# Kernel optimization log

Hardware: AMD Instinct MI355X
Metric: run time of the kernel (lower is better)

## Reference

```python
import jax, jax.numpy as jnp
import numpy as np

NUM_RANGES = 31   # bins [0,1)...[29,30) plus [30, inf) -> max_height=30
EPS = 1e-06
ALPHA = 0.5
NAN_VALUE = -1.0


def setup_inputs() -> dict:
    key = jax.random.key(0)
    k1, k2 = jax.random.split(key)
    shape = (64, 512, 512)
    # targets in log1p space; natural heights expm1(target) span [0, ~34)
    target = jax.random.uniform(k1, shape, dtype=jnp.float32) * 3.55
    pred = target + 0.1 * jax.random.normal(k2, shape, dtype=jnp.float32)
    return {"pred": pred, "target": target}


def reference(pred, target):
    valid = target != NAN_VALUE                      # no-data mask
    natural = jnp.expm1(target)                      # heights in natural space
    # arithmetic bin index: ranges [i, i+1) for i<30, last bin [30, inf)
    bin_idx = jnp.clip(jnp.floor(natural), 0.0, NUM_RANGES - 1).astype(jnp.int32)
    in_range = natural >= 0.0                        # samples below 0 fall in no range

    # histogram of valid, in-range samples (scatter-add)
    counts = jnp.zeros(NUM_RANGES, jnp.float32).at[bin_idx.ravel()].add(
        (valid & in_range).ravel().astype(jnp.float32))
    total_valid = jnp.sum(valid).astype(jnp.float32)
    denom = jnp.maximum(total_valid, 1.0)
    freq = counts / denom
    w = 1.0 / (freq ** ALPHA + EPS)                  # inverse-frequency weights, [31]

    base = jnp.abs(pred - target)                    # L1 in log1p space
    sample_w = jnp.where(in_range, w[bin_idx], 0.0)  # gather per-sample weight
    weighted = base * sample_w
    # mean over valid samples (out-of-range valid samples contribute 0, as in torch)
    mean_loss = jnp.sum(jnp.where(valid, weighted, 0.0)) / denom
    return mean_loss
```

## Files before the change

### kernel.cpp

```cpp
#include <hip/hip_runtime.h>
#include <math.h>

#define NBINS 31
#define NSLOT 32
#define NCOPIES 256
#define BLOCK 256
#define GRID 768

#define CNT_SHIFT 25
#define SUM_MASK  0x1FFFFFFu
#define FIX_SCALE 32768.0f

typedef float f4 __attribute__((ext_vector_type(4)));


__device__ __forceinline__ void prep(float p, float t, unsigned hbase,
                                     unsigned& addr, unsigned& pk, unsigned& nvalid)
{
    nvalid += (t != -1.0f) ? 1u : 0u;
    bool ok = (t >= 0.0f);
    float nat = __expf(t) - 1.0f;
    unsigned b = (unsigned)(int)fminf(nat, 30.0f);
    unsigned pkv = (1u << CNT_SHIFT)
                 | (unsigned)(fabsf(p - t) * FIX_SCALE + 0.5f);
    pk   = ok ? pkv : 0u;
    addr = hbase + ((ok ? b : 31u) << 10);
}

__device__ __forceinline__ void packet(f4 p, f4 t, unsigned hbase,
                                       unsigned& nvalid)
{
    unsigned a0, a1, a2, a3, k0, k1, k2, k3;
    prep(p.x, t.x, hbase, a0, k0, nvalid);
    prep(p.y, t.y, hbase, a1, k1, nvalid);
    prep(p.z, t.z, hbase, a2, k2, nvalid);
    prep(p.w, t.w, hbase, a3, k3, nvalid);

    unsigned r0, r1, r2, r3;
    asm volatile(
        "ds_read_b32 %0, %4\n\t"
        "ds_read_b32 %1, %5\n\t"
        "ds_read_b32 %2, %6\n\t"
        "ds_read_b32 %3, %7"
        : "=&v"(r0), "=&v"(r1), "=&v"(r2), "=&v"(r3)
        : "v"(a0), "v"(a1), "v"(a2), "v"(a3));

    unsigned s0 = k0;
    unsigned s1 = k1 + (a1 == a0 ? s0 : 0u);
    unsigned s2 = k2 + (a2 == a1 ? s1 : (a2 == a0 ? s0 : 0u));
    unsigned s3 = k3 + (a3 == a2 ? s2 : (a3 == a1 ? s1 : (a3 == a0 ? s0 : 0u)));

    asm volatile(
        "s_waitcnt lgkmcnt(0)\n\t"
        "v_add_u32 %0, %0, %4\n\t"
        "v_add_u32 %1, %1, %5\n\t"
        "v_add_u32 %2, %2, %6\n\t"
        "v_add_u32 %3, %3, %7\n\t"
        "ds_write_b32 %8, %0\n\t"
        "ds_write_b32 %9, %1\n\t"
        "ds_write_b32 %10, %2\n\t"
        "ds_write_b32 %11, %3"
        : "+v"(r0), "+v"(r1), "+v"(r2), "+v"(r3)
        : "v"(s0), "v"(s1), "v"(s2), "v"(s3),
          "v"(a0), "v"(a1), "v"(a2), "v"(a3));
}

__device__ __forceinline__ void stage(unsigned* dst, const f4* p4, const f4* t4,
                                      int idx)
{
    __builtin_amdgcn_global_load_lds(
        (const __attribute__((address_space(1))) unsigned*)(const void*)(p4 + idx),
        (__attribute__((address_space(3))) unsigned*)dst, 16, 0, 0);
    __builtin_amdgcn_global_load_lds(
        (const __attribute__((address_space(1))) unsigned*)(const void*)(t4 + idx),
        (__attribute__((address_space(3))) unsigned*)(dst + 256), 16, 0, 0);
}

__device__ __forceinline__ void unstage(unsigned sa, f4& pv, f4& tv)
{
    asm volatile(
        "ds_read_b128 %0, %2\n\t"
        "ds_read_b128 %1, %2 offset:1024\n\t"
        "s_waitcnt lgkmcnt(0)"
        : "=&v"(pv), "=&v"(tv)
        : "v"(sa));
}

__global__ __launch_bounds__(BLOCK) void zero_ws_kernel(unsigned* ws)
{
    int t = threadIdx.x;
    if (t < 192) ws[t] = 0u;
}

__global__ __launch_bounds__(BLOCK, 3) void hist_kernel(
    const float* __restrict__ pred, const float* __restrict__ target, int n,
    float* __restrict__ g_sums, unsigned* __restrict__ g_cnts,
    unsigned* __restrict__ g_total)
{
    __shared__ unsigned s_hist[NSLOT * NCOPIES];
    __shared__ unsigned s_stage[2][BLOCK / 64][512];
    __shared__ float    p_sum[NBINS * 8];
    __shared__ unsigned p_cnt[NBINS * 8];
    __shared__ unsigned s_tot[BLOCK / 64];

    const int tid = threadIdx.x;
    {
        uint4 z = make_uint4(0u, 0u, 0u, 0u);
        uint4* h4 = (uint4*)s_hist;
        #pragma unroll
        for (int k = 0; k < (NSLOT * NCOPIES / 4) / BLOCK; ++k) h4[tid + k * BLOCK] = z;
    }
    __syncthreads();

    const unsigned hbase = (unsigned)(uintptr_t)(void*)s_hist + ((unsigned)tid << 2);
    const int lane = tid & 63, wv = tid >> 6;
    unsigned* stA = &s_stage[0][wv][0];
    unsigned* stB = &s_stage[1][wv][0];
    const unsigned saA = (unsigned)(uintptr_t)(void*)stA + ((unsigned)lane << 4);
    const unsigned saB = (unsigned)(uintptr_t)(void*)stB + ((unsigned)lane << 4);
    unsigned nvalid = 0;

    const int n4 = n >> 2;
    const f4* __restrict__ pred4 = (const f4*)pred;
    const f4* __restrict__ targ4 = (const f4*)target;
    const int st = GRID * BLOCK;
    const int i0 = blockIdx.x * BLOCK + tid;

    if ((n & 3) == 0 && (n4 & 63) == 0) {
        int i = i0;
        if (i < n4) {
            stage(stA, pred4, targ4, i);
            bool curA = true;
            for (; i + st < n4; i += st) {
                if (curA) stage(stB, pred4, targ4, i + st);
                else      stage(stA, pred4, targ4, i + st);
                asm volatile("s_waitcnt vmcnt(2)" ::: "memory");
                f4 pv, tv;
                unstage(curA ? saA : saB, pv, tv);
                packet(pv, tv, hbase, nvalid);
                curA = !curA;
            }
            asm volatile("s_waitcnt vmcnt(0)" ::: "memory");
            f4 pv, tv;
            unstage(curA ? saA : saB, pv, tv);
            packet(pv, tv, hbase, nvalid);
        }
    } else {
        for (int i = i0; i < n4; i += st) {
            f4 p = pred4[i];
            f4 t = targ4[i];
            packet(p, t, hbase, nvalid);
        }
        for (int i = (n4 << 2) + i0; i < n; i += st) {
            float p = pred[i], t = target[i];
            if (t != -1.0f) {
                atomicAdd(g_total, 1u);
                if (t >= 0.0f) {
                    float nat = __expf(t) - 1.0f;
                    int b = (int)fminf(nat, 30.0f);
                    atomicAdd(&g_sums[b], fabsf(p - t));
                    atomicAdd(&g_cnts[b], 1u);
                }
            }
        }
    }
    asm volatile("s_waitcnt lgkmcnt(0)" ::: "memory");
    __syncthreads();

    if (tid < NBINS * 8) {
        const int b = tid >> 3, g = tid & 7;
        const uint4* row = (const uint4*)(s_hist + b * NCOPIES);
        float fs = 0.0f; unsigned cs = 0u;
        #pragma unroll
        for (int kk = 0; kk < 8; ++kk) {
            uint4 v = row[g + 8 * kk];
            cs += (v.x >> CNT_SHIFT) + (v.y >> CNT_SHIFT)
                + (v.z >> CNT_SHIFT) + (v.w >> CNT_SHIFT);
            fs += (float)(v.x & SUM_MASK) + (float)(v.y & SUM_MASK)
                + (float)(v.z & SUM_MASK) + (float)(v.w & SUM_MASK);
        }
        p_sum[tid] = fs;
        p_cnt[tid] = cs;
    }
    unsigned v = nvalid;
    #pragma unroll
    for (int off = 32; off >= 1; off >>= 1) v += __shfl_down(v, off, 64);
    if ((tid & 63) == 0) s_tot[tid >> 6] = v;
    __syncthreads();

    if (tid < NBINS) {
        float fs = 0.0f; unsigned cs = 0u;
        #pragma unroll
        for (int g = 0; g < 8; ++g) { fs += p_sum[tid * 8 + g]; cs += p_cnt[tid * 8 + g]; }
        atomicAdd(&g_sums[tid], fs * (1.0f / FIX_SCALE));
        atomicAdd(&g_cnts[tid], cs);
    }
    if (tid == 0) {
        unsigned tot = 0;
        #pragma unroll
        for (int w = 0; w < BLOCK / 64; ++w) tot += s_tot[w];
        atomicAdd(g_total, tot);
    }
}

__global__ void finalize_kernel(const float* __restrict__ g_sums,
                                const unsigned* __restrict__ g_cnts,
                                const unsigned* __restrict__ g_total,
                                float* __restrict__ out)
{
    int lane = threadIdx.x;
    float denom = fmaxf((float)(*g_total), 1.0f);
    float contrib = 0.0f;
    if (lane < NBINS) {
        float freq = (float)g_cnts[lane] / denom;
        float w = 1.0f / (sqrtf(freq) + 1e-6f);
        contrib = g_sums[lane] * w;
    }
    #pragma unroll
    for (int off = 32; off >= 1; off >>= 1) contrib += __shfl_down(contrib, off, 64);
    if (lane == 0) *out = contrib / denom;
}

extern "C" void kernel_launch(void* const* d_in, const int* in_sizes, int n_in,
                              void* d_out, int out_size, void* d_ws, size_t ws_size,
                              hipStream_t stream)
{
    const float* pred   = (const float*)d_in[0];
    const float* target = (const float*)d_in[1];
    float* out = (float*)d_out;
    int n = in_sizes[0];

    float*    g_sums  = (float*)d_ws;
    unsigned* g_cnts  = (unsigned*)d_ws + 64;
    unsigned* g_total = (unsigned*)d_ws + 128;

    zero_ws_kernel<<<1, BLOCK, 0, stream>>>((unsigned*)d_ws);

    hist_kernel<<<GRID, BLOCK, 0, stream>>>(pred, target, n, g_sums, g_cnts, g_total);

    finalize_kernel<<<1, 64, 0, stream>>>(g_sums, g_cnts, g_total, out);
}
```

Measured before the change: 147.7 us.

## Deepen LDS staging pipeline to four buffers and shrink grid to 512 blocks

Replaces the double-buffered global-to-LDS staging with a four-deep ring, keeping up to three loads in flight per wave with graded vmcnt waits. The grid drops from 768 to 512 blocks and the occupancy hint from 3 to 2 blocks per CU, so each thread runs more iterations and hides more latency. The packed histogram word moves to an 8-bit count field and 24-bit sum field, and the per-bin partial sums are reduced in double before the float atomic. This costs more LDS per block and lowers occupancy. The narrower count field could overflow if a histogram slot gets many hits, and the fast path now requires n4 to be a multiple of the grid stride.

```diff
diff --git a/kernel.cpp b/kernel.cpp
--- a/kernel.cpp
+++ b/kernel.cpp
@@ -5,10 +5,11 @@
 #define NSLOT 32
 #define NCOPIES 256
 #define BLOCK 256
-#define GRID 768
-
-#define CNT_SHIFT 25
-#define SUM_MASK  0x1FFFFFFu
+#define GRID 512
+#define DEPTH 4
+
+#define CNT_SHIFT 24
+#define SUM_MASK  0xFFFFFFu
 #define FIX_SCALE 32768.0f
 
 typedef float f4 __attribute__((ext_vector_type(4)));
@@ -92,13 +93,13 @@
     if (t < 192) ws[t] = 0u;
 }
 
-__global__ __launch_bounds__(BLOCK, 3) void hist_kernel(
+__global__ __launch_bounds__(BLOCK, 2) void hist_kernel(
     const float* __restrict__ pred, const float* __restrict__ target, int n,
     float* __restrict__ g_sums, unsigned* __restrict__ g_cnts,
     unsigned* __restrict__ g_total)
 {
     __shared__ unsigned s_hist[NSLOT * NCOPIES];
-    __shared__ unsigned s_stage[2][BLOCK / 64][512];
+    __shared__ unsigned s_stage[BLOCK / 64][DEPTH][512];
     __shared__ float    p_sum[NBINS * 8];
     __shared__ unsigned p_cnt[NBINS * 8];
     __shared__ unsigned s_tot[BLOCK / 64];
@@ -114,10 +115,8 @@
 
     const unsigned hbase = (unsigned)(uintptr_t)(void*)s_hist + ((unsigned)tid << 2);
     const int lane = tid & 63, wv = tid >> 6;
-    unsigned* stA = &s_stage[0][wv][0];
-    unsigned* stB = &s_stage[1][wv][0];
-    const unsigned saA = (unsigned)(uintptr_t)(void*)stA + ((unsigned)lane << 4);
-    const unsigned saB = (unsigned)(uintptr_t)(void*)stB + ((unsigned)lane << 4);
+    unsigned* wb = &s_stage[wv][0][0];
+    const unsigned sbase = (unsigned)(uintptr_t)(void*)wb + ((unsigned)lane << 4);
     unsigned nvalid = 0;
 
     const int n4 = n >> 2;
@@ -125,24 +124,26 @@
     const f4* __restrict__ targ4 = (const f4*)target;
     const int st = GRID * BLOCK;
     const int i0 = blockIdx.x * BLOCK + tid;
-
-    if ((n & 3) == 0 && (n4 & 63) == 0) {
-        int i = i0;
-        if (i < n4) {
-            stage(stA, pred4, targ4, i);
-            bool curA = true;
-            for (; i + st < n4; i += st) {
-                if (curA) stage(stB, pred4, targ4, i + st);
-                else      stage(stA, pred4, targ4, i + st);
+    const int T  = n4 / st;
+
+    if ((n & 3) == 0 && (n4 % st) == 0 && T >= DEPTH) {
+        stage(wb,        pred4, targ4, i0);
+        stage(wb + 512,  pred4, targ4, i0 + st);
+        stage(wb + 1024, pred4, targ4, i0 + 2 * st);
+        int i = i0 + 3 * st;
+        for (int k = 0; k < T; ++k, i += st) {
+            if (k + 3 < T) {
+                stage(wb + ((unsigned)((k + 3) & 3) << 9), pred4, targ4, i);
+                asm volatile("s_waitcnt vmcnt(6)" ::: "memory");
+            } else if (k + 2 < T) {
+                asm volatile("s_waitcnt vmcnt(4)" ::: "memory");
+            } else if (k + 1 < T) {
                 asm volatile("s_waitcnt vmcnt(2)" ::: "memory");
-                f4 pv, tv;
-                unstage(curA ? saA : saB, pv, tv);
-                packet(pv, tv, hbase, nvalid);
-                curA = !curA;
+            } else {
+                asm volatile("s_waitcnt vmcnt(0)" ::: "memory");
             }
-            asm volatile("s_waitcnt vmcnt(0)" ::: "memory");
             f4 pv, tv;
-            unstage(curA ? saA : saB, pv, tv);
+            unstage(sbase + ((unsigned)(k & 3) << 11), pv, tv);
             packet(pv, tv, hbase, nvalid);
         }
     } else {
@@ -189,10 +190,10 @@
     __syncthreads();
 
     if (tid < NBINS) {
-        float fs = 0.0f; unsigned cs = 0u;
-        #pragma unroll
-        for (int g = 0; g < 8; ++g) { fs += p_sum[tid * 8 + g]; cs += p_cnt[tid * 8 + g]; }
-        atomicAdd(&g_sums[tid], fs * (1.0f / FIX_SCALE));
+        double fs = 0.0; unsigned cs = 0u;
+        #pragma unroll
+        for (int g = 0; g < 8; ++g) { fs += (double)p_sum[tid * 8 + g]; cs += p_cnt[tid * 8 + g]; }
+        atomicAdd(&g_sums[tid], (float)(fs * (1.0 / (double)FIX_SCALE)));
         atomicAdd(&g_cnts[tid], cs);
     }
     if (tid == 0) {
```

Result: no change. 148.8 us (+0.8%).
